# Performance work log

Measured on AMD Instinct MI355X. Metric: run time of the kernel, lower is better.

Reference implementation:

```python
import jax, jax.numpy as jnp
import numpy as np

N_NODES = 100000
N_EDGES = 3200000
FEAT = 64
N_GRAPHS = 64


def setup_inputs() -> dict:
    key = jax.random.key(0)
    ks = jax.random.split(key, 6)
    x = jax.random.normal(ks[0], (N_NODES, FEAT), dtype=jnp.float32)
    edge_index = jax.random.randint(ks[1], (2, N_EDGES), 0, N_NODES, dtype=jnp.int64)
    batch = jnp.sort(jax.random.randint(ks[2], (N_NODES,), 0, N_GRAPHS, dtype=jnp.int64))
    W1 = jax.random.normal(ks[3], (FEAT, FEAT), dtype=jnp.float32) * 0.1
    b1 = jnp.zeros((FEAT,), dtype=jnp.float32)
    W2 = jax.random.normal(ks[4], (FEAT, FEAT), dtype=jnp.float32) * 0.1
    b2 = jnp.zeros((FEAT,), dtype=jnp.float32)
    return {"x": x, "edge_index": edge_index, "batch": batch,
            "W1": W1, "b1": b1, "W2": W2, "b2": b2}


def _gcn_conv(x, W, b, row, col, n_nodes):
    # GCNConv: x' = D^{-1/2} (A + I) D^{-1/2} (x W) + b  (self-loops already in row/col)
    h = x @ W                                               # [N, F_out]
    deg = jax.ops.segment_sum(jnp.ones_like(col, dtype=h.dtype), col,
                              num_segments=n_nodes)         # [N]
    dinv = jnp.where(deg > 0, jax.lax.rsqrt(deg), 0.0)
    norm = dinv[row] * dinv[col]                            # [E+N]
    msgs = h[row] * norm[:, None]                           # gather + scale  [E+N, F]
    out = jax.ops.segment_sum(msgs, col, num_segments=n_nodes)  # scatter-add
    return out + b


def reference(x, edge_index, batch, W1, b1, W2, b2):
    n_nodes = x.shape[0]
    # add self-loops (PyG GCNConv default)
    loop = jnp.arange(n_nodes, dtype=edge_index.dtype)
    row = jnp.concatenate([edge_index[0], loop])
    col = jnp.concatenate([edge_index[1], loop])

    h = _gcn_conv(x, W1, b1, row, col, n_nodes)
    h = jax.nn.relu(h)
    # dropout is identity in eval mode (deterministic reference)
    h = _gcn_conv(h, W2, b2, row, col, n_nodes)
    h = jax.nn.relu(h)

    # global mean pool over graphs in the batch
    sums = jax.ops.segment_sum(h, batch, num_segments=N_GRAPHS)          # [G, F]
    counts = jax.ops.segment_sum(jnp.ones((n_nodes,), h.dtype), batch,
                                 num_segments=N_GRAPHS)                  # [G]
    return sums / jnp.maximum(counts, 1.0)[:, None]
```

## Files before the change

kernel.cpp:

```cpp
#include <hip/hip_runtime.h>

#define N_NODES 100000
#define N_EDGES 3200000
#define FEAT 64
#define N_GRAPHS 64

#define BKT_SHIFT 9
#define BKT_SIZE  512
#define NBKT      196
#define BKT_PAD   20000
#define E4        (N_EDGES / 4)

__device__ __forceinline__ ushort f2bf(float f) {
    unsigned u = __float_as_uint(f);
    return (ushort)((u + 0x7fffu + ((u >> 16) & 1u)) >> 16);
}
__device__ __forceinline__ float bf2f(ushort s) {
    return __uint_as_float(((unsigned)s) << 16);
}

__global__ void k_zero(int* __restrict__ bcnt, float* __restrict__ pool, int* __restrict__ offs) {
    int i = blockIdx.x * blockDim.x + threadIdx.x;
    if (i < NBKT) bcnt[i] = 0;
    if (i < N_GRAPHS * FEAT + N_GRAPHS) pool[i] = 0.0f;
    if (i == 0) offs[N_NODES] = N_EDGES;
}

__global__ void __launch_bounds__(1024) k_bucket(const int* __restrict__ row,
                                                 const int* __restrict__ col,
                                                 int* __restrict__ bcnt,
                                                 int* __restrict__ tmp) {
    __shared__ int lcnt[NBKT];
    int tid = threadIdx.x;
    if (tid < NBKT) lcnt[tid] = 0;
    __syncthreads();
    int base = blockIdx.x * 4096;
    #pragma unroll
    for (int k = 0; k < 4; ++k) {
        int t4 = base + k * 1024 + tid;
        if (t4 < E4) {
            int4 c = ((const int4*)col)[t4];
            atomicAdd(&lcnt[c.x >> BKT_SHIFT], 1);
            atomicAdd(&lcnt[c.y >> BKT_SHIFT], 1);
            atomicAdd(&lcnt[c.z >> BKT_SHIFT], 1);
            atomicAdd(&lcnt[c.w >> BKT_SHIFT], 1);
        }
    }
    __syncthreads();
    if (tid < NBKT) lcnt[tid] = atomicAdd(&bcnt[tid], lcnt[tid]);
    __syncthreads();
    #pragma unroll
    for (int k = 0; k < 4; ++k) {
        int t4 = base + k * 1024 + tid;
        if (t4 < E4) {
            int4 c = ((const int4*)col)[t4];
            int4 r = ((const int4*)row)[t4];
            int b0 = c.x >> BKT_SHIFT, b1 = c.y >> BKT_SHIFT, b2 = c.z >> BKT_SHIFT, b3 = c.w >> BKT_SHIFT;
            int s0 = atomicAdd(&lcnt[b0], 1);
            int s1 = atomicAdd(&lcnt[b1], 1);
            int s2 = atomicAdd(&lcnt[b2], 1);
            int s3 = atomicAdd(&lcnt[b3], 1);
            tmp[b0 * BKT_PAD + s0] = (r.x << BKT_SHIFT) | (c.x & (BKT_SIZE - 1));
            tmp[b1 * BKT_PAD + s1] = (r.y << BKT_SHIFT) | (c.y & (BKT_SIZE - 1));
            tmp[b2 * BKT_PAD + s2] = (r.z << BKT_SHIFT) | (c.z & (BKT_SIZE - 1));
            tmp[b3 * BKT_PAD + s3] = (r.w << BKT_SHIFT) | (c.w & (BKT_SIZE - 1));
        }
    }
}

__global__ void __launch_bounds__(512) k_build(const int* __restrict__ tmp,
                                               const int* __restrict__ bcnt,
                                               int* __restrict__ offs,
                                               float* __restrict__ dinv,
                                               int* __restrict__ csr_row) {
    __shared__ int segl[BKT_PAD];
    __shared__ int hist[BKT_SIZE];
    __shared__ int wpart[8];
    __shared__ int sh_start;
    int b = blockIdx.x, tid = threadIdx.x;

    if (tid < 64) {
        int sum = 0;
        for (int c = 0; c < NBKT; c += 64) {
            int idx = c + tid;
            int v = (idx < b) ? bcnt[idx] : 0;
            #pragma unroll
            for (int d2 = 1; d2 < 64; d2 <<= 1) v += __shfl_xor(v, d2);
            sum += v;
        }
        if (tid == 0) sh_start = sum;
    }
    if (tid < BKT_SIZE) hist[tid] = 0;
    __syncthreads();
    int s = sh_start;
    int count = min(bcnt[b], BKT_PAD);
    const int* seg = tmp + (size_t)b * BKT_PAD;

    for (int i = tid; i < count; i += 512) {
        int v = seg[i];
        segl[i] = v;
        atomicAdd(&hist[v & (BKT_SIZE - 1)], 1);
    }
    __syncthreads();

    int cnt_n = hist[tid];
    int p = cnt_n;
    #pragma unroll
    for (int d = 1; d < 64; d <<= 1) {
        int t2 = __shfl_up(p, d);
        if ((tid & 63) >= d) p += t2;
    }
    if ((tid & 63) == 63) wpart[tid >> 6] = p;
    __syncthreads();
    if (tid == 0) {
        int run = 0;
        #pragma unroll
        for (int w = 0; w < 8; ++w) { int t2 = wpart[w]; wpart[w] = run; run += t2; }
    }
    __syncthreads();
    int excl = wpart[tid >> 6] + p - cnt_n;
    int node = (b << BKT_SHIFT) + tid;
    if (node < N_NODES) {
        offs[node] = s + excl;
        dinv[node] = rsqrtf((float)(cnt_n + 1));
    }
    hist[tid] = s + excl;
    __syncthreads();

    for (int i = tid; i < count; i += 512) {
        int v = segl[i];
        int slot = atomicAdd(&hist[v & (BKT_SIZE - 1)], 1);
        csr_row[slot] = v >> BKT_SHIFT;
    }
}

template <bool TRANS>
__global__ void __launch_bounds__(256, 4) k_gemm(const void* __restrict__ in_,
                                                 const float* __restrict__ W,
                                                 const float* __restrict__ bias,
                                                 const float* __restrict__ dinv,
                                                 ushort* __restrict__ out) {
    __shared__ float Ws[64][64];
    __shared__ float At[64][68];
    int tid = threadIdx.x;
    int row0 = blockIdx.x * 64;

    const float4* Wv = (const float4*)W;
    #pragma unroll
    for (int i = 0; i < 4; ++i) {
        int idx = tid + i * 256;
        float4 v = Wv[idx];
        *(float4*)&Ws[idx >> 4][(idx & 15) * 4] = v;
    }
    if constexpr (TRANS) {
        const ushort* in = (const ushort*)in_;
        #pragma unroll
        for (int i = 0; i < 2; ++i) {
            int idx = tid + i * 256;
            int r = idx >> 3, q = idx & 7;
            int grow = row0 + r;
            uint4 v = make_uint4(0u, 0u, 0u, 0u);
            if (grow < N_NODES) v = ((const uint4*)(in + (size_t)grow * FEAT))[q];
            float4 b0 = ((const float4*)bias)[q * 2];
            float4 b1 = ((const float4*)bias)[q * 2 + 1];
            int k = q * 8;
            At[k + 0][r] = fmaxf(__uint_as_float(v.x << 16)          + b0.x, 0.f);
            At[k + 1][r] = fmaxf(__uint_as_float(v.x & 0xffff0000u)  + b0.y, 0.f);
            At[k + 2][r] = fmaxf(__uint_as_float(v.y << 16)          + b0.z, 0.f);
            At[k + 3][r] = fmaxf(__uint_as_float(v.y & 0xffff0000u)  + b0.w, 0.f);
            At[k + 4][r] = fmaxf(__uint_as_float(v.z << 16)          + b1.x, 0.f);
            At[k + 5][r] = fmaxf(__uint_as_float(v.z & 0xffff0000u)  + b1.y, 0.f);
            At[k + 6][r] = fmaxf(__uint_as_float(v.w << 16)          + b1.z, 0.f);
            At[k + 7][r] = fmaxf(__uint_as_float(v.w & 0xffff0000u)  + b1.w, 0.f);
        }
    } else {
        const float* in = (const float*)in_;
        #pragma unroll
        for (int i = 0; i < 4; ++i) {
            int idx = tid + i * 256;
            int r = idx >> 4, f4 = idx & 15;
            int grow = row0 + r;
            float4 v = make_float4(0.f, 0.f, 0.f, 0.f);
            if (grow < N_NODES) v = ((const float4*)(in + (size_t)grow * FEAT))[f4];
            int k = f4 * 4;
            At[k][r] = v.x; At[k + 1][r] = v.y; At[k + 2][r] = v.z; At[k + 3][r] = v.w;
        }
    }
    __syncthreads();

    int tx = tid & 15, ty = tid >> 4;
    float acc[4][4] = {};
    #pragma unroll 8
    for (int k = 0; k < 64; ++k) {
        float4 wv = *(const float4*)&Ws[k][tx * 4];
        float4 av = *(const float4*)&At[k][ty * 4];
        acc[0][0] = fmaf(av.x, wv.x, acc[0][0]); acc[0][1] = fmaf(av.x, wv.y, acc[0][1]);
        acc[0][2] = fmaf(av.x, wv.z, acc[0][2]); acc[0][3] = fmaf(av.x, wv.w, acc[0][3]);
        acc[1][0] = fmaf(av.y, wv.x, acc[1][0]); acc[1][1] = fmaf(av.y, wv.y, acc[1][1]);
        acc[1][2] = fmaf(av.y, wv.z, acc[1][2]); acc[1][3] = fmaf(av.y, wv.w, acc[1][3]);
        acc[2][0] = fmaf(av.z, wv.x, acc[2][0]); acc[2][1] = fmaf(av.z, wv.y, acc[2][1]);
        acc[2][2] = fmaf(av.z, wv.z, acc[2][2]); acc[2][3] = fmaf(av.z, wv.w, acc[2][3]);
        acc[3][0] = fmaf(av.w, wv.x, acc[3][0]); acc[3][1] = fmaf(av.w, wv.y, acc[3][1]);
        acc[3][2] = fmaf(av.w, wv.z, acc[3][2]); acc[3][3] = fmaf(av.w, wv.w, acc[3][3]);
    }
    #pragma unroll
    for (int i = 0; i < 4; ++i) {
        int r = row0 + ty * 4 + i;
        if (r < N_NODES) {
            float d = dinv[r];
            ushort4 o;
            o.x = f2bf(acc[i][0] * d);
            o.y = f2bf(acc[i][1] * d);
            o.z = f2bf(acc[i][2] * d);
            o.w = f2bf(acc[i][3] * d);
            *(ushort4*)(out + (size_t)r * FEAT + tx * 4) = o;
        }
    }
}

__global__ void k_gather(const ushort* __restrict__ h, const float* __restrict__ dinv,
                         const int* __restrict__ off, const int* __restrict__ csr_row,
                         ushort* __restrict__ out) {
    int tid = threadIdx.x;
    int lane = tid & 63;
    int node = blockIdx.x * (blockDim.x >> 6) + (tid >> 6);
    if (node >= N_NODES) return;
    int g = lane >> 3;
    int sl = lane & 7;
    int s = off[node], e = off[node + 1];
    float a0 = 0.f, a1 = 0.f, a2 = 0.f, a3 = 0.f, a4 = 0.f, a5 = 0.f, a6 = 0.f, a7 = 0.f;

#define ACC8(v) do {                                         \
        a0 += __uint_as_float((v).x << 16);                  \
        a1 += __uint_as_float((v).x & 0xffff0000u);          \
        a2 += __uint_as_float((v).y << 16);                  \
        a3 += __uint_as_float((v).y & 0xffff0000u);          \
        a4 += __uint_as_float((v).z << 16);                  \
        a5 += __uint_as_float((v).z & 0xffff0000u);          \
        a6 += __uint_as_float((v).w << 16);                  \
        a7 += __uint_as_float((v).w & 0xffff0000u);          \
    } while (0)

    if (g == 0) {
        uint4 v = ((const uint4*)(h + (size_t)node * FEAT))[sl];
        ACC8(v);
    }
    int base = s;
    for (; base + 32 <= e; base += 32) {
        int r0 = csr_row[base + g];
        int r1 = csr_row[base + 8 + g];
        int r2 = csr_row[base + 16 + g];
        int r3 = csr_row[base + 24 + g];
        uint4 v0 = ((const uint4*)(h + (size_t)r0 * FEAT))[sl];
        uint4 v1 = ((const uint4*)(h + (size_t)r1 * FEAT))[sl];
        uint4 v2 = ((const uint4*)(h + (size_t)r2 * FEAT))[sl];
        uint4 v3 = ((const uint4*)(h + (size_t)r3 * FEAT))[sl];
        ACC8(v0); ACC8(v1); ACC8(v2); ACC8(v3);
    }
    for (; base < e; base += 8) {
        int ei = base + g;
        if (ei < e) {
            int r = csr_row[ei];
            uint4 v = ((const uint4*)(h + (size_t)r * FEAT))[sl];
            ACC8(v);
        }
    }
#undef ACC8
#define RED(a) a += __shfl_xor(a, 8); a += __shfl_xor(a, 16); a += __shfl_xor(a, 32);
    RED(a0) RED(a1) RED(a2) RED(a3) RED(a4) RED(a5) RED(a6) RED(a7)
#undef RED
    if (g == 0) {
        float d = dinv[node];
        uint4 o;
        o.x = (unsigned)f2bf(a0 * d) | ((unsigned)f2bf(a1 * d) << 16);
        o.y = (unsigned)f2bf(a2 * d) | ((unsigned)f2bf(a3 * d) << 16);
        o.z = (unsigned)f2bf(a4 * d) | ((unsigned)f2bf(a5 * d) << 16);
        o.w = (unsigned)f2bf(a6 * d) | ((unsigned)f2bf(a7 * d) << 16);
        ((uint4*)(out + (size_t)node * FEAT))[sl] = o;
    }
}

__global__ void k_pool(const ushort* __restrict__ agg, const float* __restrict__ b2,
                       const int* __restrict__ batch, float* sums, float* cnts) {
    const int NPB = 64;
    int f = threadIdx.x;
    int start = blockIdx.x * NPB;
    if (start >= N_NODES) return;
    int end = min(start + NPB, N_NODES);
    float bias = b2[f];
    int gcur = batch[start];
    float acc = 0.0f, cacc = 0.0f;
    for (int n = start; n < end; ++n) {
        int g = batch[n];
        if (g != gcur) {
            atomicAdd(&sums[gcur * FEAT + f], acc);
            if (f == 0) atomicAdd(&cnts[gcur], cacc);
            acc = 0.0f; cacc = 0.0f; gcur = g;
        }
        float v = bf2f(agg[(size_t)n * FEAT + f]) + bias;
        acc += fmaxf(v, 0.0f);
        cacc += 1.0f;
    }
    atomicAdd(&sums[gcur * FEAT + f], acc);
    if (f == 0) atomicAdd(&cnts[gcur], cacc);
}

__global__ void k_final(const float* __restrict__ sums, const float* __restrict__ cnts,
                        float* __restrict__ out) {
    int i = blockIdx.x * blockDim.x + threadIdx.x;
    if (i < N_GRAPHS * FEAT) out[i] = sums[i] / fmaxf(cnts[i >> 6], 1.0f);
}

extern "C" void kernel_launch(void* const* d_in, const int* in_sizes, int n_in,
                              void* d_out, int out_size, void* d_ws, size_t ws_size,
                              hipStream_t stream) {
    const float* x     = (const float*)d_in[0];
    const int*   ei    = (const int*)d_in[1];
    const int*   batch = (const int*)d_in[2];
    const float* W1    = (const float*)d_in[3];
    const float* b1    = (const float*)d_in[4];
    const float* W2    = (const float*)d_in[5];
    const float* b2    = (const float*)d_in[6];
    const int* row = ei;
    const int* col = ei + N_EDGES;

    size_t o = 0;
    auto alloc = [&](size_t bytes) { size_t cur = o; o = (o + bytes + 255) & ~(size_t)255; return cur; };
    char* ws = (char*)d_ws;
    float*  dinv    = (float*) (ws + alloc(N_NODES * 4));
    int*    offs    = (int*)   (ws + alloc((N_NODES + 1) * 4));
    int*    bcnt    = (int*)   (ws + alloc(NBKT * 4));
    float*  pool    = (float*) (ws + alloc((N_GRAPHS * FEAT + N_GRAPHS) * 4));
    ushort* hbf     = (ushort*)(ws + alloc((size_t)N_NODES * FEAT * 2));
    ushort* aggA    = (ushort*)(ws + alloc((size_t)N_NODES * FEAT * 2));
    ushort* aggB    = (ushort*)(ws + alloc((size_t)N_NODES * FEAT * 2));
    int*    csr_row = (int*)   (ws + alloc((size_t)N_EDGES * 4));
    int*    tmp     = (int*)   (ws + alloc((size_t)NBKT * BKT_PAD * 4));
    float* psum = pool;
    float* pcnt = pool + N_GRAPHS * FEAT;

    const int B = 256;
    hipLaunchKernelGGL(k_zero, dim3(17), dim3(B), 0, stream, bcnt, pool, offs);
    hipLaunchKernelGGL(k_bucket, dim3(196), dim3(1024), 0, stream, row, col, bcnt, tmp);
    hipLaunchKernelGGL(k_build, dim3(NBKT), dim3(512), 0, stream, tmp, bcnt, offs, dinv, csr_row);

    hipLaunchKernelGGL((k_gemm<false>), dim3((N_NODES + 63) / 64), dim3(B), 0, stream, (const void*)x, W1, b1, dinv, hbf);
    hipLaunchKernelGGL(k_gather, dim3((N_NODES + 3) / 4), dim3(B), 0, stream, hbf, dinv, offs, csr_row, aggA);
    hipLaunchKernelGGL((k_gemm<true>), dim3((N_NODES + 63) / 64), dim3(B), 0, stream, (const void*)aggA, W2, b1, dinv, hbf);
    hipLaunchKernelGGL(k_gather, dim3((N_NODES + 3) / 4), dim3(B), 0, stream, hbf, dinv, offs, csr_row, aggB);

    hipLaunchKernelGGL(k_pool, dim3((N_NODES + 63) / 64), dim3(64), 0, stream, aggB, b2, batch, psum, pcnt);
    hipLaunchKernelGGL(k_final, dim3(16), dim3(B), 0, stream, psum, pcnt, (float*)d_out);
}
```

Baseline: 243.3 us.

## Fuse layer-1 GEMM into edge bucketing kernel and move source scaling into gather

Result: faster. 233.7 us (-4.0%).

```diff
diff --git a/kernel.cpp b/kernel.cpp
--- a/kernel.cpp
+++ b/kernel.cpp
@@ -5,11 +5,12 @@
 #define FEAT 64
 #define N_GRAPHS 64
 
-#define BKT_SHIFT 9
-#define BKT_SIZE  512
-#define NBKT      196
-#define BKT_PAD   20000
+#define BKT_SHIFT 8
+#define BKT_SIZE  256
+#define NBKT      391
+#define BKT_PAD   8960
 #define E4        (N_EDGES / 4)
+#define GEMM1_BLKS ((N_NODES + 63) / 64)
 
 __device__ __forceinline__ ushort f2bf(float f) {
     unsigned u = __float_as_uint(f);
@@ -26,56 +27,95 @@
     if (i == 0) offs[N_NODES] = N_EDGES;
 }
 
-__global__ void __launch_bounds__(1024) k_bucket(const int* __restrict__ row,
-                                                 const int* __restrict__ col,
-                                                 int* __restrict__ bcnt,
-                                                 int* __restrict__ tmp) {
+__global__ void __launch_bounds__(1024) k_pre(const int* __restrict__ row,
+                                              const int* __restrict__ col,
+                                              int* __restrict__ bcnt,
+                                              int* __restrict__ tmp,
+                                              const float* __restrict__ x,
+                                              const float* __restrict__ W1,
+                                              ushort* __restrict__ hbf) {
     __shared__ int lcnt[NBKT];
+    __shared__ float Ws[64][64];
+    __shared__ float At[64][68];
     int tid = threadIdx.x;
-    if (tid < NBKT) lcnt[tid] = 0;
-    __syncthreads();
-    int base = blockIdx.x * 4096;
-    #pragma unroll
-    for (int k = 0; k < 4; ++k) {
-        int t4 = base + k * 1024 + tid;
-        if (t4 < E4) {
-            int4 c = ((const int4*)col)[t4];
-            atomicAdd(&lcnt[c.x >> BKT_SHIFT], 1);
-            atomicAdd(&lcnt[c.y >> BKT_SHIFT], 1);
-            atomicAdd(&lcnt[c.z >> BKT_SHIFT], 1);
-            atomicAdd(&lcnt[c.w >> BKT_SHIFT], 1);
-        }
-    }
-    __syncthreads();
-    if (tid < NBKT) lcnt[tid] = atomicAdd(&bcnt[tid], lcnt[tid]);
-    __syncthreads();
-    #pragma unroll
-    for (int k = 0; k < 4; ++k) {
-        int t4 = base + k * 1024 + tid;
-        if (t4 < E4) {
-            int4 c = ((const int4*)col)[t4];
-            int4 r = ((const int4*)row)[t4];
-            int b0 = c.x >> BKT_SHIFT, b1 = c.y >> BKT_SHIFT, b2 = c.z >> BKT_SHIFT, b3 = c.w >> BKT_SHIFT;
-            int s0 = atomicAdd(&lcnt[b0], 1);
-            int s1 = atomicAdd(&lcnt[b1], 1);
-            int s2 = atomicAdd(&lcnt[b2], 1);
-            int s3 = atomicAdd(&lcnt[b3], 1);
-            tmp[b0 * BKT_PAD + s0] = (r.x << BKT_SHIFT) | (c.x & (BKT_SIZE - 1));
-            tmp[b1 * BKT_PAD + s1] = (r.y << BKT_SHIFT) | (c.y & (BKT_SIZE - 1));
-            tmp[b2 * BKT_PAD + s2] = (r.z << BKT_SHIFT) | (c.z & (BKT_SIZE - 1));
-            tmp[b3 * BKT_PAD + s3] = (r.w << BKT_SHIFT) | (c.w & (BKT_SIZE - 1));
-        }
-    }
-}
-
-__global__ void __launch_bounds__(512) k_build(const int* __restrict__ tmp,
-                                               const int* __restrict__ bcnt,
-                                               int* __restrict__ offs,
-                                               float* __restrict__ dinv,
-                                               int* __restrict__ csr_row) {
-    __shared__ int segl[BKT_PAD];
+
+    if (blockIdx.x < 196) {
+        if (tid < NBKT) lcnt[tid] = 0;
+        __syncthreads();
+        int base = blockIdx.x * 4096;
+        int4 c[4];
+        #pragma unroll
+        for (int k = 0; k < 4; ++k) {
+            int t4 = base + k * 1024 + tid;
+            if (t4 < E4) {
+                c[k] = ((const int4*)col)[t4];
+                atomicAdd(&lcnt[c[k].x >> BKT_SHIFT], 1);
+                atomicAdd(&lcnt[c[k].y >> BKT_SHIFT], 1);
+                atomicAdd(&lcnt[c[k].z >> BKT_SHIFT], 1);
+                atomicAdd(&lcnt[c[k].w >> BKT_SHIFT], 1);
+            }
+        }
+        __syncthreads();
+        if (tid < NBKT) lcnt[tid] = atomicAdd(&bcnt[tid], lcnt[tid]);
+        __syncthreads();
+        #pragma unroll
+        for (int k = 0; k < 4; ++k) {
+            int t4 = base + k * 1024 + tid;
+            if (t4 < E4) {
+                int4 r = ((const int4*)row)[t4];
+                int b0 = c[k].x >> BKT_SHIFT, b1 = c[k].y >> BKT_SHIFT;
+                int b2 = c[k].z >> BKT_SHIFT, b3 = c[k].w >> BKT_SHIFT;
+                int s0 = atomicAdd(&lcnt[b0], 1);
+                int s1 = atomicAdd(&lcnt[b1], 1);
+                int s2 = atomicAdd(&lcnt[b2], 1);
+                int s3 = atomicAdd(&lcnt[b3], 1);
+                if (s0 < BKT_PAD) tmp[b0 * BKT_PAD + s0] = (r.x << BKT_SHIFT) | (c[k].x & (BKT_SIZE - 1));
+                if (s1 < BKT_PAD) tmp[b1 * BKT_PAD + s1] = (r.y << BKT_SHIFT) | (c[k].y & (BKT_SIZE - 1));
+                if (s2 < BKT_PAD) tmp[b2 * BKT_PAD + s2] = (r.z << BKT_SHIFT) | (c[k].z & (BKT_SIZE - 1));
+                if (s3 < BKT_PAD) tmp[b3 * BKT_PAD + s3] = (r.w << BKT_SHIFT) | (c[k].w & (BKT_SIZE - 1));
+            }
+        }
+    } else {
+        int row0 = (blockIdx.x - 196) * 64;
+        {
+            float4 v = ((const float4*)W1)[tid];
+            *(float4*)&Ws[tid >> 4][(tid & 15) * 4] = v;
+        }
+        {
+            int r = tid >> 4, f4 = tid & 15;
+            int grow = row0 + r;
+            float4 v = make_float4(0.f, 0.f, 0.f, 0.f);
+            if (grow < N_NODES) v = ((const float4*)(x + (size_t)grow * FEAT))[f4];
+            int k = f4 * 4;
+            At[k][r] = v.x; At[k + 1][r] = v.y; At[k + 2][r] = v.z; At[k + 3][r] = v.w;
+        }
+        __syncthreads();
+        int tx = tid & 31, ty = tid >> 5;
+        float a00 = 0.f, a01 = 0.f, a10 = 0.f, a11 = 0.f;
+        #pragma unroll 8
+        for (int k = 0; k < 64; ++k) {
+            float2 wv = *(const float2*)&Ws[k][tx * 2];
+            float2 av = *(const float2*)&At[k][ty * 2];
+            a00 = fmaf(av.x, wv.x, a00); a01 = fmaf(av.x, wv.y, a01);
+            a10 = fmaf(av.y, wv.x, a10); a11 = fmaf(av.y, wv.y, a11);
+        }
+        int r0 = row0 + ty * 2;
+        if (r0 < N_NODES)
+            *(unsigned*)(hbf + (size_t)r0 * FEAT + tx * 2) =
+                (unsigned)f2bf(a00) | ((unsigned)f2bf(a01) << 16);
+        if (r0 + 1 < N_NODES)
+            *(unsigned*)(hbf + (size_t)(r0 + 1) * FEAT + tx * 2) =
+                (unsigned)f2bf(a10) | ((unsigned)f2bf(a11) << 16);
+    }
+}
+
+__global__ void __launch_bounds__(1024) k_build(const int* __restrict__ tmp,
+                                                const int* __restrict__ bcnt,
+                                                int* __restrict__ offs,
+                                                float* __restrict__ dinv,
+                                                int* __restrict__ csr_row) {
     __shared__ int hist[BKT_SIZE];
-    __shared__ int wpart[8];
+    __shared__ int wpart[4];
     __shared__ int sh_start;
     int b = blockIdx.x, tid = threadIdx.x;
 
@@ -96,50 +136,61 @@
     int count = min(bcnt[b], BKT_PAD);
     const int* seg = tmp + (size_t)b * BKT_PAD;
 
-    for (int i = tid; i < count; i += 512) {
-        int v = seg[i];
-        segl[i] = v;
-        atomicAdd(&hist[v & (BKT_SIZE - 1)], 1);
-    }
-    __syncthreads();
-
-    int cnt_n = hist[tid];
-    int p = cnt_n;
+    int e[9];
     #pragma unroll
-    for (int d = 1; d < 64; d <<= 1) {
-        int t2 = __shfl_up(p, d);
-        if ((tid & 63) >= d) p += t2;
-    }
-    if ((tid & 63) == 63) wpart[tid >> 6] = p;
+    for (int k = 0; k < 9; ++k) {
+        int idx = k * 1024 + tid;
+        e[k] = -1;
+        if (idx < count) {
+            e[k] = seg[idx];
+            atomicAdd(&hist[e[k] & (BKT_SIZE - 1)], 1);
+        }
+    }
+    __syncthreads();
+
+    int cnt_n = 0, p = 0;
+    if (tid < BKT_SIZE) {
+        cnt_n = hist[tid];
+        p = cnt_n;
+        #pragma unroll
+        for (int d = 1; d < 64; d <<= 1) {
+            int t2 = __shfl_up(p, d);
+            if ((tid & 63) >= d) p += t2;
+        }
+        if ((tid & 63) == 63) wpart[tid >> 6] = p;
+    }
     __syncthreads();
     if (tid == 0) {
         int run = 0;
         #pragma unroll
-        for (int w = 0; w < 8; ++w) { int t2 = wpart[w]; wpart[w] = run; run += t2; }
-    }
-    __syncthreads();
-    int excl = wpart[tid >> 6] + p - cnt_n;
-    int node = (b << BKT_SHIFT) + tid;
-    if (node < N_NODES) {
-        offs[node] = s + excl;
-        dinv[node] = rsqrtf((float)(cnt_n + 1));
-    }
-    hist[tid] = s + excl;
-    __syncthreads();
-
-    for (int i = tid; i < count; i += 512) {
-        int v = segl[i];
-        int slot = atomicAdd(&hist[v & (BKT_SIZE - 1)], 1);
-        csr_row[slot] = v >> BKT_SHIFT;
-    }
-}
-
-template <bool TRANS>
-__global__ void __launch_bounds__(256, 4) k_gemm(const void* __restrict__ in_,
-                                                 const float* __restrict__ W,
-                                                 const float* __restrict__ bias,
-                                                 const float* __restrict__ dinv,
-                                                 ushort* __restrict__ out) {
+        for (int w = 0; w < 4; ++w) { int t2 = wpart[w]; wpart[w] = run; run += t2; }
+    }
+    __syncthreads();
+    if (tid < BKT_SIZE) {
+        int excl = wpart[tid >> 6] + p - cnt_n;
+        int node = (b << BKT_SHIFT) + tid;
+        if (node < N_NODES) {
+            offs[node] = s + excl;
+            dinv[node] = rsqrtf((float)(cnt_n + 1));
+        }
+        hist[tid] = s + excl;
+    }
+    __syncthreads();
+
+    #pragma unroll
+    for (int k = 0; k < 9; ++k) {
+        if (e[k] >= 0) {
+            int slot = atomicAdd(&hist[e[k] & (BKT_SIZE - 1)], 1);
+            csr_row[slot] = e[k] >> BKT_SHIFT;
+        }
+    }
+}
+
+__global__ void __launch_bounds__(256, 4) k_gemm2(const ushort* __restrict__ in,
+                                                  const float* __restrict__ W,
+                                                  const float* __restrict__ bias,
+                                                  const float* __restrict__ dinv,
+                                                  ushort* __restrict__ out) {
     __shared__ float Ws[64][64];
     __shared__ float At[64][68];
     int tid = threadIdx.x;
@@ -152,39 +203,24 @@
         float4 v = Wv[idx];
         *(float4*)&Ws[idx >> 4][(idx & 15) * 4] = v;
     }
-    if constexpr (TRANS) {
-        const ushort* in = (const ushort*)in_;
-        #pragma unroll
-        for (int i = 0; i < 2; ++i) {
-            int idx = tid + i * 256;
-            int r = idx >> 3, q = idx & 7;
-            int grow = row0 + r;
-            uint4 v = make_uint4(0u, 0u, 0u, 0u);
-            if (grow < N_NODES) v = ((const uint4*)(in + (size_t)grow * FEAT))[q];
-            float4 b0 = ((const float4*)bias)[q * 2];
-            float4 b1 = ((const float4*)bias)[q * 2 + 1];
-            int k = q * 8;
-            At[k + 0][r] = fmaxf(__uint_as_float(v.x << 16)          + b0.x, 0.f);
-            At[k + 1][r] = fmaxf(__uint_as_float(v.x & 0xffff0000u)  + b0.y, 0.f);
-            At[k + 2][r] = fmaxf(__uint_as_float(v.y << 16)          + b0.z, 0.f);
-            At[k + 3][r] = fmaxf(__uint_as_float(v.y & 0xffff0000u)  + b0.w, 0.f);
-            At[k + 4][r] = fmaxf(__uint_as_float(v.z << 16)          + b1.x, 0.f);
-            At[k + 5][r] = fmaxf(__uint_as_float(v.z & 0xffff0000u)  + b1.y, 0.f);
-            At[k + 6][r] = fmaxf(__uint_as_float(v.w << 16)          + b1.z, 0.f);
-            At[k + 7][r] = fmaxf(__uint_as_float(v.w & 0xffff0000u)  + b1.w, 0.f);
-        }
-    } else {
-        const float* in = (const float*)in_;
-        #pragma unroll
-        for (int i = 0; i < 4; ++i) {
-            int idx = tid + i * 256;
-            int r = idx >> 4, f4 = idx & 15;
-            int grow = row0 + r;
-            float4 v = make_float4(0.f, 0.f, 0.f, 0.f);
-            if (grow < N_NODES) v = ((const float4*)(in + (size_t)grow * FEAT))[f4];
-            int k = f4 * 4;
-            At[k][r] = v.x; At[k + 1][r] = v.y; At[k + 2][r] = v.z; At[k + 3][r] = v.w;
-        }
+    #pragma unroll
+    for (int i = 0; i < 2; ++i) {
+        int idx = tid + i * 256;
+        int r = idx >> 3, q = idx & 7;
+        int grow = row0 + r;
+        uint4 v = make_uint4(0u, 0u, 0u, 0u);
+        if (grow < N_NODES) v = ((const uint4*)(in + (size_t)grow * FEAT))[q];
+        float4 b0 = ((const float4*)bias)[q * 2];
+        float4 b1 = ((const float4*)bias)[q * 2 + 1];
+        int k = q * 8;
+        At[k + 0][r] = fmaxf(__uint_as_float(v.x << 16)          + b0.x, 0.f);
+        At[k + 1][r] = fmaxf(__uint_as_float(v.x & 0xffff0000u)  + b0.y, 0.f);
+        At[k + 2][r] = fmaxf(__uint_as_float(v.y << 16)          + b0.z, 0.f);
+        At[k + 3][r] = fmaxf(__uint_as_float(v.y & 0xffff0000u)  + b0.w, 0.f);
+        At[k + 4][r] = fmaxf(__uint_as_float(v.z << 16)          + b1.x, 0.f);
+        At[k + 5][r] = fmaxf(__uint_as_float(v.z & 0xffff0000u)  + b1.y, 0.f);
+        At[k + 6][r] = fmaxf(__uint_as_float(v.w << 16)          + b1.z, 0.f);
+        At[k + 7][r] = fmaxf(__uint_as_float(v.w & 0xffff0000u)  + b1.w, 0.f);
     }
     __syncthreads();
 
@@ -218,6 +254,7 @@
     }
 }
 
+template <bool SRC_SCALED>
 __global__ void k_gather(const ushort* __restrict__ h, const float* __restrict__ dinv,
                          const int* __restrict__ off, const int* __restrict__ csr_row,
                          ushort* __restrict__ out) {
@@ -230,20 +267,21 @@
     int s = off[node], e = off[node + 1];
     float a0 = 0.f, a1 = 0.f, a2 = 0.f, a3 = 0.f, a4 = 0.f, a5 = 0.f, a6 = 0.f, a7 = 0.f;
 
-#define ACC8(v) do {                                         \
-        a0 += __uint_as_float((v).x << 16);                  \
-        a1 += __uint_as_float((v).x & 0xffff0000u);          \
-        a2 += __uint_as_float((v).y << 16);                  \
-        a3 += __uint_as_float((v).y & 0xffff0000u);          \
-        a4 += __uint_as_float((v).z << 16);                  \
-        a5 += __uint_as_float((v).z & 0xffff0000u);          \
-        a6 += __uint_as_float((v).w << 16);                  \
-        a7 += __uint_as_float((v).w & 0xffff0000u);          \
+#define ACC8(vv, wt) do {                                           \
+        a0 = fmaf(__uint_as_float((vv).x << 16),         wt, a0);   \
+        a1 = fmaf(__uint_as_float((vv).x & 0xffff0000u), wt, a1);   \
+        a2 = fmaf(__uint_as_float((vv).y << 16),         wt, a2);   \
+        a3 = fmaf(__uint_as_float((vv).y & 0xffff0000u), wt, a3);   \
+        a4 = fmaf(__uint_as_float((vv).z << 16),         wt, a4);   \
+        a5 = fmaf(__uint_as_float((vv).z & 0xffff0000u), wt, a5);   \
+        a6 = fmaf(__uint_as_float((vv).w << 16),         wt, a6);   \
+        a7 = fmaf(__uint_as_float((vv).w & 0xffff0000u), wt, a7);   \
     } while (0)
 
+    float selfw = SRC_SCALED ? 1.0f : dinv[node];
     if (g == 0) {
         uint4 v = ((const uint4*)(h + (size_t)node * FEAT))[sl];
-        ACC8(v);
+        ACC8(v, selfw);
     }
     int base = s;
     for (; base + 32 <= e; base += 32) {
@@ -251,18 +289,33 @@
         int r1 = csr_row[base + 8 + g];
         int r2 = csr_row[base + 16 + g];
         int r3 = csr_row[base + 24 + g];
+        float w0 = SRC_SCALED ? 1.0f : dinv[r0];
+        float w1 = SRC_SCALED ? 1.0f : dinv[r1];
+        float w2 = SRC_SCALED ? 1.0f : dinv[r2];
+        float w3 = SRC_SCALED ? 1.0f : dinv[r3];
         uint4 v0 = ((const uint4*)(h + (size_t)r0 * FEAT))[sl];
         uint4 v1 = ((const uint4*)(h + (size_t)r1 * FEAT))[sl];
         uint4 v2 = ((const uint4*)(h + (size_t)r2 * FEAT))[sl];
         uint4 v3 = ((const uint4*)(h + (size_t)r3 * FEAT))[sl];
-        ACC8(v0); ACC8(v1); ACC8(v2); ACC8(v3);
+        ACC8(v0, w0); ACC8(v1, w1); ACC8(v2, w2); ACC8(v3, w3);
+    }
+    if (base + 16 <= e) {
+        int r0 = csr_row[base + g];
+        int r1 = csr_row[base + 8 + g];
+        float w0 = SRC_SCALED ? 1.0f : dinv[r0];
+        float w1 = SRC_SCALED ? 1.0f : dinv[r1];
+        uint4 v0 = ((const uint4*)(h + (size_t)r0 * FEAT))[sl];
+        uint4 v1 = ((const uint4*)(h + (size_t)r1 * FEAT))[sl];
+        ACC8(v0, w0); ACC8(v1, w1);
+        base += 16;
     }
     for (; base < e; base += 8) {
         int ei = base + g;
         if (ei < e) {
             int r = csr_row[ei];
+            float wt = SRC_SCALED ? 1.0f : dinv[r];
             uint4 v = ((const uint4*)(h + (size_t)r * FEAT))[sl];
-            ACC8(v);
+            ACC8(v, wt);
         }
     }
 #undef ACC8
@@ -341,13 +394,15 @@
 
     const int B = 256;
     hipLaunchKernelGGL(k_zero, dim3(17), dim3(B), 0, stream, bcnt, pool, offs);
-    hipLaunchKernelGGL(k_bucket, dim3(196), dim3(1024), 0, stream, row, col, bcnt, tmp);
-    hipLaunchKernelGGL(k_build, dim3(NBKT), dim3(512), 0, stream, tmp, bcnt, offs, dinv, csr_row);
-
-    hipLaunchKernelGGL((k_gemm<false>), dim3((N_NODES + 63) / 64), dim3(B), 0, stream, (const void*)x, W1, b1, dinv, hbf);
-    hipLaunchKernelGGL(k_gather, dim3((N_NODES + 3) / 4), dim3(B), 0, stream, hbf, dinv, offs, csr_row, aggA);
-    hipLaunchKernelGGL((k_gemm<true>), dim3((N_NODES + 63) / 64), dim3(B), 0, stream, (const void*)aggA, W2, b1, dinv, hbf);
-    hipLaunchKernelGGL(k_gather, dim3((N_NODES + 3) / 4), dim3(B), 0, stream, hbf, dinv, offs, csr_row, aggB);
+    hipLaunchKernelGGL(k_pre, dim3(196 + GEMM1_BLKS), dim3(1024), 0, stream,
+                       row, col, bcnt, tmp, x, W1, hbf);
+    hipLaunchKernelGGL(k_build, dim3(NBKT), dim3(1024), 0, stream, tmp, bcnt, offs, dinv, csr_row);
+
+    hipLaunchKernelGGL((k_gather<false>), dim3((N_NODES + 3) / 4), dim3(B), 0, stream,
+                       hbf, dinv, offs, csr_row, aggA);
+    hipLaunchKernelGGL(k_gemm2, dim3((N_NODES + 63) / 64), dim3(B), 0, stream, aggA, W2, b1, dinv, hbf);
+    hipLaunchKernelGGL((k_gather<true>), dim3((N_NODES + 3) / 4), dim3(B), 0, stream,
+                       hbf, dinv, offs, csr_row, aggB);
 
     hipLaunchKernelGGL(k_pool, dim3((N_NODES + 63) / 64), dim3(64), 0, stream, aggB, b2, batch, psum, pcnt);
     hipLaunchKernelGGL(k_final, dim3(16), dim3(B), 0, stream, psum, pcnt, (float*)d_out);
```
